# Optimization experiments

Measured on AMD Instinct MI355X. Metric: run time of the kernel, lower is better.

Reference implementation:

```python
import jax, jax.numpy as jnp
import numpy as np

HIDDEN = 256
NUM_CLASSES = 25
INPUT_DIM = 76


def _lstm_layer(x, Wi, Wh, b):
    """Flax OptimizedLSTMCell semantics: gates [i, f, g, o], zero-init carry.
    x: [B, T, D]; Wi: [D, 4H]; Wh: [H, 4H]; b: [4H]. Returns hidden seq [B, T, H]."""
    B = x.shape[0]
    H = Wh.shape[0]
    c0 = jnp.zeros((B, H), x.dtype)
    h0 = jnp.zeros((B, H), x.dtype)

    def step(carry, xt):
        c, h = carry
        z = xt @ Wi + h @ Wh + b  # [B, 4H]
        i, f, g, o = jnp.split(z, 4, axis=-1)
        i = jax.nn.sigmoid(i)
        f = jax.nn.sigmoid(f)
        g = jnp.tanh(g)
        o = jax.nn.sigmoid(o)
        c = f * c + i * g
        h = o * jnp.tanh(c)
        return (c, h), h

    (_, _), ys = jax.lax.scan(step, (c0, h0), jnp.swapaxes(x, 0, 1))  # scan over time
    return jnp.swapaxes(ys, 0, 1)  # [B, T, H]


def setup_inputs() -> dict:
    key = jax.random.key(0)
    ks = jax.random.split(key, 9)
    B, T, D, H = 512, 512, INPUT_DIM, HIDDEN
    s_in = 1.0 / np.sqrt(D)
    s_h = 1.0 / np.sqrt(H)
    return {
        "x": jax.random.normal(ks[0], (B, T, D), jnp.float32),
        "Wi1": jax.random.normal(ks[1], (D, 4 * H), jnp.float32) * s_in,
        "Wh1": jax.random.normal(ks[2], (H, 4 * H), jnp.float32) * s_h,
        "b1": jnp.zeros((4 * H,), jnp.float32),
        "Wi2": jax.random.normal(ks[3], (H, 4 * H), jnp.float32) * s_h,
        "Wh2": jax.random.normal(ks[4], (H, 4 * H), jnp.float32) * s_h,
        "b2": jnp.zeros((4 * H,), jnp.float32),
        "Wd": jax.random.normal(ks[5], (H, NUM_CLASSES), jnp.float32) * s_h,
        "bd": jnp.zeros((NUM_CLASSES,), jnp.float32),
    }


def reference(x, Wi1, Wh1, b1, Wi2, Wh2, b2, Wd, bd):
    h1 = _lstm_layer(x, Wi1, Wh1, b1)   # [B, T, H]
    h2 = _lstm_layer(h1, Wi2, Wh2, b2)  # [B, T, H]
    feats = h2[:, -1]                   # dropout deterministic (eval mode)
    logits = feats @ Wd + bd            # [B, num_classes]
    return logits
```

## Files before the change

kernel.cpp:

```cpp
#include <hip/hip_runtime.h>

#define BB 512
#define TT 512
#define DD 76
#define HH 256
#define NC 25
#define NBLK 256
#define NTHREADS 512
#define BBHH (BB * HH)

#define K1 352
#define K2 512
#define WS1 360
#define WS2 520

typedef unsigned short u16;
typedef unsigned int u32;
typedef unsigned long long u64;
typedef __attribute__((ext_vector_type(8))) short bf16x8;
typedef __attribute__((ext_vector_type(4))) float f32x4;

__device__ __forceinline__ float bf2f(u16 v) {
  union { u32 u; float f; } c; c.u = ((u32)v) << 16; return c.f;
}
__device__ __forceinline__ u16 f2bf(float f) {
  union { u32 u; float f; } c; c.f = f;
  u32 r = c.u + 0x7FFFu + ((c.u >> 16) & 1u);
  return (u16)(r >> 16);
}
__device__ __forceinline__ void split2(float f, u16& h, u16& l) {
  u16 hh = f2bf(f);
  float r = f - bf2f(hh);
  h = hh; l = f2bf(r);
}
__device__ __forceinline__ float tanh_f(float v) {
  float e = __expf(2.0f * v);
  return 1.0f - 2.0f / (e + 1.0f);
}
__device__ __forceinline__ float gact(float v, bool is_tanh) {
  float e = __expf(is_tanh ? 2.0f * v : -v);
  float inv = 1.0f / (1.0f + e);
  return is_tanh ? 1.0f - 2.0f * inv : inv;
}

__device__ __forceinline__ u64 ald2(const u32* p) {
  return __hip_atomic_load((const u64*)p, __ATOMIC_RELAXED, __HIP_MEMORY_SCOPE_AGENT);
}
__device__ __forceinline__ u32 ald1(const u32* p) {
  return __hip_atomic_load(p, __ATOMIC_RELAXED, __HIP_MEMORY_SCOPE_AGENT);
}
__device__ __forceinline__ void ast1(u32* p, u32 v) {
  __hip_atomic_store(p, v, __ATOMIC_RELAXED, __HIP_MEMORY_SCOPE_AGENT);
}
__device__ __forceinline__ void ast2(u64* p, u64 v) {
  __hip_atomic_store(p, v, __ATOMIC_RELAXED, __HIP_MEMORY_SCOPE_AGENT);
}

__device__ __forceinline__ void wait_flags(const u32* fbase, u32 target) {
  if (threadIdx.x < 32) {
    const u32* p = fbase + threadIdx.x * 32;
    while (__hip_atomic_load(p, __ATOMIC_RELAXED, __HIP_MEMORY_SCOPE_AGENT) < target)
      __builtin_amdgcn_s_sleep(1);
  }
  __syncthreads();
}
__device__ __forceinline__ void post_flag(u32* slot, u32 val) {
  __syncthreads();
  if (threadIdx.x == 0) ast1(slot, val);
}

__device__ __forceinline__ bf16x8 hi8(const u64 w[4]) {
  union { u32 u[4]; bf16x8 v; } c;
#pragma unroll
  for (int i = 0; i < 4; ++i)
    c.u[i] = __builtin_amdgcn_perm((u32)(w[i] >> 32), (u32)w[i], 0x05040100u);
  return c.v;
}
__device__ __forceinline__ bf16x8 lo8(const u64 w[4]) {
  union { u32 u[4]; bf16x8 v; } c;
#pragma unroll
  for (int i = 0; i < 4; ++i)
    c.u[i] = __builtin_amdgcn_perm((u32)(w[i] >> 32), (u32)w[i], 0x07060302u);
  return c.v;
}

__device__ __forceinline__ void splitv8(const float* f, bf16x8& vh, bf16x8& vl) {
  union { u16 s[8]; bf16x8 v; } ch, cl;
#pragma unroll
  for (int i = 0; i < 8; ++i) { u16 h_, l_; split2(f[i], h_, l_); ch.s[i] = h_; cl.s[i] = l_; }
  vh = ch.v; vl = cl.v;
}

__global__ void repack_kernel(const float* __restrict__ Wi1, const float* __restrict__ Wh1,
                              const float* __restrict__ Wi2, const float* __restrict__ Wh2,
                              u16* __restrict__ w1hg, u16* __restrict__ w1lg,
                              u16* __restrict__ w2hg, u16* __restrict__ w2lg) {
  int idx = blockIdx.x * blockDim.x + threadIdx.x;
  const int N1 = 1024 * K1;
  if (idx < N1) {
    int c = idx / K1, k = idx - c * K1;
    int src = (c & 3) * HH + (c >> 2);
    float v = 0.f;
    if (k < HH) v = Wh1[k * 1024 + src];
    else if (k < HH + DD) v = Wi1[(k - HH) * 1024 + src];
    u16 h, l; split2(v, h, l);
    w1hg[idx] = h; w1lg[idx] = l;
  } else if (idx < N1 + 1024 * K2) {
    int d = idx - N1;
    int c = d >> 9, k = d & 511;
    int src = (c & 3) * HH + (c >> 2);
    float v = (k < HH) ? Wi2[k * 1024 + src] : Wh2[(k - HH) * 1024 + src];
    u16 h, l; split2(v, h, l);
    w2hg[d] = h; w2lg[d] = l;
  }
}

#define MFMA_CH6(AH, AL, PH0, PL0, PH1, PL1, KOFF, A0, B0, C0, A1, B1, C1)  \
  { bf16x8 b0h_ = *(const bf16x8*)((PH0) + (KOFF));                         \
    bf16x8 b0l_ = *(const bf16x8*)((PL0) + (KOFF));                         \
    bf16x8 b1h_ = *(const bf16x8*)((PH1) + (KOFF));                         \
    bf16x8 b1l_ = *(const bf16x8*)((PL1) + (KOFF));                         \
    A0 = __builtin_amdgcn_mfma_f32_16x16x32_bf16(AH, b0h_, A0, 0, 0, 0);    \
    B0 = __builtin_amdgcn_mfma_f32_16x16x32_bf16(AH, b0l_, B0, 0, 0, 0);    \
    C0 = __builtin_amdgcn_mfma_f32_16x16x32_bf16(AL, b0h_, C0, 0, 0, 0);    \
    A1 = __builtin_amdgcn_mfma_f32_16x16x32_bf16(AH, b1h_, A1, 0, 0, 0);    \
    B1 = __builtin_amdgcn_mfma_f32_16x16x32_bf16(AH, b1l_, B1, 0, 0, 0);    \
    C1 = __builtin_amdgcn_mfma_f32_16x16x32_bf16(AL, b1h_, C1, 0, 0, 0); }

#define GATES_ST(Z, CS, DST)                                                \
  { u32 hwv[4];                                                             \
    _Pragma("unroll")                                                       \
    for (int r = 0; r < 4; ++r) {                                           \
      float a_ = gact((Z)[r], gi == 2);                                     \
      float v1_ = __shfl_xor(a_, 1);                                        \
      float v2_ = __shfl_xor(a_, 2);                                        \
      float v3_ = __shfl_xor(a_, 3);                                        \
      float cn_ = v1_ * (CS)[r] + a_ * v2_;                                 \
      (CS)[r] = cn_;                                                        \
      float hv_ = v3_ * tanh_f(cn_);                                        \
      u16 hh_, hl_; split2(hv_, hh_, hl_);                                  \
      hwv[r] = (u32)hh_ | ((u32)hl_ << 16);                                 \
    }                                                                       \
    _Pragma("unroll")                                                       \
    for (int r = 0; r < 4; ++r) {                                           \
      int base_ = lane & 48;                                                \
      u32 w1_ = __shfl(hwv[r], base_ + 4);                                  \
      u32 w2_ = __shfl(hwv[r], base_ + 8);                                  \
      u32 w3_ = __shfl(hwv[r], base_ + 12);                                 \
      if (nl == 0) {                                                        \
        u64* dp_ = (u64*)((DST) + (size_t)(rbase + r) * HH + jt * 8 + kh * 4); \
        ast2(dp_,     (u64)hwv[r] | ((u64)w1_ << 32));                      \
        ast2(dp_ + 1, (u64)w2_    | ((u64)w3_ << 32));                      \
      }                                                                     \
    }                                                                       \
  }

#define LOAD_RW(RW, BASEPTR)                                                \
  { const u32* hp_ = (BASEPTR) + (size_t)arow * HH + kh * 128;              \
    _Pragma("unroll")                                                       \
    for (int i_ = 0; i_ < 4; ++i_) {                                        \
      const u32* p_ = hp_ + i_ * 32 + qd * 8;                               \
      (RW)[i_][0] = ald2(p_);     (RW)[i_][1] = ald2(p_ + 2);               \
      (RW)[i_][2] = ald2(p_ + 4); (RW)[i_][3] = ald2(p_ + 6);               \
    } }

__global__ __launch_bounds__(NTHREADS) void lstm_kernel(
    const float* __restrict__ x,
    const float* __restrict__ b1, const float* __restrict__ b2,
    const float* __restrict__ Wd, const float* __restrict__ bd,
    const u16* __restrict__ w1hg, const u16* __restrict__ w1lg,
    const u16* __restrict__ w2hg, const u16* __restrict__ w2lg,
    u32* __restrict__ h1w, u32* __restrict__ h2w,
    u32* __restrict__ flags,
    float* __restrict__ out)
{
  __shared__ u16 w1h[32 * WS1], w1l[32 * WS1];
  __shared__ u16 w2h[32 * WS2], w2l[32 * WS2];
  __shared__ float zx[2][8][64][4];

  const int tid = threadIdx.x;
  const int lane = tid & 63;
  const int wv = tid >> 6;
  const int m  = wv & 3;
  const int kh = wv >> 2;
  const int nl = lane & 15;
  const int qd = lane >> 4;
  const int bt = blockIdx.x & 7;
  const int jt = blockIdx.x >> 3;
  const int row0 = bt * 64;

  u32* fCp = flags + bt * 1024;
  u32* fCslot = fCp + jt * 32;

  for (int i = tid; i < 32 * (K1 / 2); i += NTHREADS) {
    int c = i / 176, kk = i - c * 176;
    ((u32*)&w1h[c * WS1])[kk] = ((const u32*)(w1hg + (size_t)(jt * 32 + c) * K1))[kk];
    ((u32*)&w1l[c * WS1])[kk] = ((const u32*)(w1lg + (size_t)(jt * 32 + c) * K1))[kk];
  }
  for (int i = tid; i < 32 * (K2 / 2); i += NTHREADS) {
    int c = i >> 8, kk = i & 255;
    ((u32*)&w2h[c * WS2])[kk] = ((const u32*)(w2hg + (size_t)(jt * 32 + c) * K2))[kk];
    ((u32*)&w2l[c * WS2])[kk] = ((const u32*)(w2lg + (size_t)(jt * 32 + c) * K2))[kk];
  }

  const int cg_col = jt * 32 + kh * 16 + nl;
  const int gi = cg_col & 3;
  const int rbase = row0 + m * 16 + qd * 4;
  const int arow = row0 + m * 16 + nl;

  float ab1[2], ab2[2];
#pragma unroll
  for (int tl = 0; tl < 2; ++tl) {
    int col = jt * 32 + tl * 16 + nl;
    float v1 = b1[(col & 3) * HH + (col >> 2)];
    float v2 = b2[(col & 3) * HH + (col >> 2)];
    ab1[tl] = (kh == 0) ? v1 : 0.f;
    ab2[tl] = (kh == 0) ? v2 : 0.f;
  }

  const u16* pB1h0 = w1h + nl * WS1;
  const u16* pB1l0 = w1l + nl * WS1;
  const u16* pB1h1 = w1h + (16 + nl) * WS1;
  const u16* pB1l1 = w1l + (16 + nl) * WS1;
  const u16* pB2h0 = w2h + nl * WS2;
  const u16* pB2l0 = w2l + nl * WS2;
  const u16* pB2h1 = w2h + (16 + nl) * WS2;
  const u16* pB2l1 = w2l + (16 + nl) * WS2;

  float cs1[4] = {0.f, 0.f, 0.f, 0.f}, cs2[4] = {0.f, 0.f, 0.f, 0.f};
  u64 rwh1[4][4], rw2[4][4];

  __syncthreads();

  {
    f32x4 aA0 = {ab1[0], ab1[0], ab1[0], ab1[0]};
    f32x4 aA1 = {ab1[1], ab1[1], ab1[1], ab1[1]};
    f32x4 aB0 = {0,0,0,0}, aB1 = {0,0,0,0}, aC0 = {0,0,0,0}, aC1 = {0,0,0,0};
    const float* xrow = x + (size_t)arow * TT * DD;
    if (kh == 0) {
#pragma unroll
      for (int ci = 0; ci < 2; ++ci) {
        float xv[8];
        float4 f0 = *(const float4*)(xrow + ci * 32 + qd * 8);
        float4 f1 = *(const float4*)(xrow + ci * 32 + qd * 8 + 4);
        xv[0]=f0.x; xv[1]=f0.y; xv[2]=f0.z; xv[3]=f0.w;
        xv[4]=f1.x; xv[5]=f1.y; xv[6]=f1.z; xv[7]=f1.w;
        bf16x8 xh, xl; splitv8(xv, xh, xl);
        const int koff = (8 + ci) * 32 + qd * 8;
        MFMA_CH6(xh, xl, pB1h0, pB1l0, pB1h1, pB1l1, koff, aA0, aB0, aC0, aA1, aB1, aC1)
      }
    } else {
      float xv[8] = {0,0,0,0,0,0,0,0};
      if (qd == 0) {
        float4 f0 = *(const float4*)(xrow + 64);
        float4 f1 = *(const float4*)(xrow + 68);
        xv[0]=f0.x; xv[1]=f0.y; xv[2]=f0.z; xv[3]=f0.w;
        xv[4]=f1.x; xv[5]=f1.y; xv[6]=f1.z; xv[7]=f1.w;
      } else if (qd == 1) {
        float4 f0 = *(const float4*)(xrow + 72);
        xv[0]=f0.x; xv[1]=f0.y; xv[2]=f0.z; xv[3]=f0.w;
      }
      bf16x8 xh, xl; splitv8(xv, xh, xl);
      const int koff = 10 * 32 + qd * 8;
      MFMA_CH6(xh, xl, pB1h0, pB1l0, pB1h1, pB1l1, koff, aA0, aB0, aC0, aA1, aB1, aC1)
    }
    f32x4 zk = (kh == 0) ? (aA0 + aB0 + aC0) : (aA1 + aB1 + aC1);
    f32x4 zo = (kh == 0) ? (aA1 + aB1 + aC1) : (aA0 + aB0 + aC0);
    *(f32x4*)&zx[1][wv][lane][0] = zo;
    __syncthreads();
    zk += *(const f32x4*)&zx[1][wv ^ 4][lane][0];
    GATES_ST(zk, cs1, h1w)
    post_flag(fCslot, 1u);
  }

#pragma unroll 1
  for (int t = 0; t < TT; ++t) {
    const u32* h1cw = h1w + (t & 1) * BBHH;
    u32* h1nw = h1w + ((t + 1) & 1) * BBHH;
    const u32* h2pw = h2w + ((t + 1) & 1) * BBHH;
    u32* h2cw = h2w + (t & 1) * BBHH;
    const bool doA = (t < TT - 1);

    f32x4 aA0 = {ab1[0], ab1[0], ab1[0], ab1[0]};
    f32x4 aA1 = {ab1[1], ab1[1], ab1[1], ab1[1]};
    f32x4 aB0 = {0,0,0,0}, aB1 = {0,0,0,0}, aC0 = {0,0,0,0}, aC1 = {0,0,0,0};
    f32x4 bA0 = {ab2[0], ab2[0], ab2[0], ab2[0]};
    f32x4 bA1 = {ab2[1], ab2[1], ab2[1], ab2[1]};
    f32x4 bB0 = {0,0,0,0}, bB1 = {0,0,0,0}, bC0 = {0,0,0,0}, bC1 = {0,0,0,0};

    float4 xf0, xf1, xf2, xf3;
    if (doA) {
      const float* xrow = x + ((size_t)arow * TT + (t + 1)) * DD;
      if (kh == 0) {
        xf0 = *(const float4*)(xrow + qd * 8);
        xf1 = *(const float4*)(xrow + qd * 8 + 4);
        xf2 = *(const float4*)(xrow + 32 + qd * 8);
        xf3 = *(const float4*)(xrow + 32 + qd * 8 + 4);
      } else {
        xf0 = make_float4(0,0,0,0); xf1 = make_float4(0,0,0,0);
        if (qd == 0) {
          xf0 = *(const float4*)(xrow + 64);
          xf1 = *(const float4*)(xrow + 68);
        } else if (qd == 1) {
          xf0 = *(const float4*)(xrow + 72);
        }
      }
    }

    wait_flags(fCp, (u32)(t + 1));

    LOAD_RW(rwh1, h1cw)
    if (t > 0) LOAD_RW(rw2, h2pw)

    if (doA) {
      float xv[8]; bf16x8 xh, xl;
      if (kh == 0) {
        xv[0]=xf0.x; xv[1]=xf0.y; xv[2]=xf0.z; xv[3]=xf0.w;
        xv[4]=xf1.x; xv[5]=xf1.y; xv[6]=xf1.z; xv[7]=xf1.w;
        splitv8(xv, xh, xl);
        MFMA_CH6(xh, xl, pB1h0, pB1l0, pB1h1, pB1l1, 8 * 32 + qd * 8,
                 aA0, aB0, aC0, aA1, aB1, aC1)
        xv[0]=xf2.x; xv[1]=xf2.y; xv[2]=xf2.z; xv[3]=xf2.w;
        xv[4]=xf3.x; xv[5]=xf3.y; xv[6]=xf3.z; xv[7]=xf3.w;
        splitv8(xv, xh, xl);
        MFMA_CH6(xh, xl, pB1h0, pB1l0, pB1h1, pB1l1, 9 * 32 + qd * 8,
                 aA0, aB0, aC0, aA1, aB1, aC1)
      } else {
        xv[0]=xf0.x; xv[1]=xf0.y; xv[2]=xf0.z; xv[3]=xf0.w;
        xv[4]=xf1.x; xv[5]=xf1.y; xv[6]=xf1.z; xv[7]=xf1.w;
        splitv8(xv, xh, xl);
        MFMA_CH6(xh, xl, pB1h0, pB1l0, pB1h1, pB1l1, 10 * 32 + qd * 8,
                 aA0, aB0, aC0, aA1, aB1, aC1)
      }
    }

#pragma unroll
    for (int i = 0; i < 4; ++i) {
      bf16x8 fh = hi8(rwh1[i]), fl = lo8(rwh1[i]);
      const int koff = (kh * 4 + i) * 32 + qd * 8;
      if (doA)
        MFMA_CH6(fh, fl, pB1h0, pB1l0, pB1h1, pB1l1, koff, aA0, aB0, aC0, aA1, aB1, aC1)
      MFMA_CH6(fh, fl, pB2h0, pB2l0, pB2h1, pB2l1, koff, bA0, bB0, bC0, bA1, bB1, bC1)
    }
    if (t > 0) {
#pragma unroll
      for (int i = 0; i < 4; ++i) {
        bf16x8 fh = hi8(rw2[i]), fl = lo8(rw2[i]);
        const int koff = (8 + kh * 4 + i) * 32 + qd * 8;
        MFMA_CH6(fh, fl, pB2h0, pB2l0, pB2h1, pB2l1, koff, bA0, bB0, bC0, bA1, bB1, bC1)
      }
    }

    f32x4 z2k = (kh == 0) ? (bA0 + bB0 + bC0) : (bA1 + bB1 + bC1);
    f32x4 z2o = (kh == 0) ? (bA1 + bB1 + bC1) : (bA0 + bB0 + bC0);
    *(f32x4*)&zx[0][wv][lane][0] = z2o;
    f32x4 z1k = {0,0,0,0};
    if (doA) {
      z1k = (kh == 0) ? (aA0 + aB0 + aC0) : (aA1 + aB1 + aC1);
      f32x4 z1o = (kh == 0) ? (aA1 + aB1 + aC1) : (aA0 + aB0 + aC0);
      *(f32x4*)&zx[1][wv][lane][0] = z1o;
    }
    __syncthreads();
    z2k += *(const f32x4*)&zx[0][wv ^ 4][lane][0];
    if (doA) {
      z1k += *(const f32x4*)&zx[1][wv ^ 4][lane][0];
      GATES_ST(z1k, cs1, h1nw)
    }
    GATES_ST(z2k, cs2, h2cw)
    post_flag(fCslot, (u32)(t + 2));
  }

  wait_flags(fCp, TT + 1);
  if (tid < 2 * NC) {
    int r = row0 + jt * 2 + tid / NC;
    int n = tid - (tid / NC) * NC;
    float s = bd[n];
    const u32* fw = h2w + BBHH + (size_t)r * HH;
#pragma unroll 8
    for (int k = 0; k < HH; ++k) {
      u32 w = ald1(fw + k);
      s += (bf2f((u16)w) + bf2f((u16)(w >> 16))) * Wd[k * NC + n];
    }
    out[r * NC + n] = s;
  }
}

extern "C" void kernel_launch(void* const* d_in, const int* in_sizes, int n_in,
                              void* d_out, int out_size, void* d_ws, size_t ws_size,
                              hipStream_t stream) {
  const float* x   = (const float*)d_in[0];
  const float* Wi1 = (const float*)d_in[1];
  const float* Wh1 = (const float*)d_in[2];
  const float* b1  = (const float*)d_in[3];
  const float* Wi2 = (const float*)d_in[4];
  const float* Wh2 = (const float*)d_in[5];
  const float* b2  = (const float*)d_in[6];
  const float* Wd  = (const float*)d_in[7];
  const float* bd  = (const float*)d_in[8];

  char* ws = (char*)d_ws;
  u32* h1w = (u32*)(ws);
  u32* h2w = (u32*)(ws + 1048576u);
  u16* w1hg = (u16*)(ws + 2097152u);
  u16* w1lg = (u16*)(ws + 2097152u + 720896u);
  u16* w2hg = (u16*)(ws + 2097152u + 2u * 720896u);
  u16* w2lg = (u16*)(ws + 2097152u + 2u * 720896u + 1048576u);
  u32* flags = (u32*)(ws + 5636096u);
  float* out = (float*)d_out;

  hipMemsetAsync((void*)flags, 0, 65536, stream);
  const int total = 1024 * K1 + 1024 * K2;
  repack_kernel<<<(total + 255) / 256, 256, 0, stream>>>(
      Wi1, Wh1, Wi2, Wh2, w1hg, w1lg, w2hg, w2lg);

  void* args[] = {
    (void*)&x, (void*)&b1, (void*)&b2, (void*)&Wd, (void*)&bd,
    (void*)&w1hg, (void*)&w1lg, (void*)&w2hg, (void*)&w2lg,
    (void*)&h1w, (void*)&h2w,
    (void*)&flags, (void*)&out
  };
  (void)hipLaunchCooperativeKernel((void*)lstm_kernel, dim3(NBLK),
                                   dim3(NTHREADS), args, 0, stream);
}
```

Measured before the change: 5.481 ms.

## Split columns across waves instead of K to remove LDS reduction and barrier

Each wave now computes the full K reduction for one 16-column tile instead of half of K for two tiles. This removes the shared-memory partial-sum exchange and its __syncthreads. Every wave polls the inter-block flags itself, so the barrier after the wait is dropped. Before the flag is published, an explicit vmcnt wait ensures the h stores have completed. In exchange, each wave loads twice as many h values from global memory, holds more registers, and adds redundant flag polling.

```diff
diff --git a/kernel.cpp b/kernel.cpp
--- a/kernel.cpp
+++ b/kernel.cpp
@@ -56,17 +56,13 @@
   __hip_atomic_store(p, v, __ATOMIC_RELAXED, __HIP_MEMORY_SCOPE_AGENT);
 }
 
-__device__ __forceinline__ void wait_flags(const u32* fbase, u32 target) {
-  if (threadIdx.x < 32) {
-    const u32* p = fbase + threadIdx.x * 32;
+__device__ __forceinline__ void wwait(const u32* fbase, u32 target) {
+  if ((threadIdx.x & 63) < 32) {
+    const u32* p = fbase + (threadIdx.x & 63) * 32;
     while (__hip_atomic_load(p, __ATOMIC_RELAXED, __HIP_MEMORY_SCOPE_AGENT) < target)
       __builtin_amdgcn_s_sleep(1);
   }
-  __syncthreads();
-}
-__device__ __forceinline__ void post_flag(u32* slot, u32 val) {
-  __syncthreads();
-  if (threadIdx.x == 0) ast1(slot, val);
+  asm volatile("" ::: "memory");
 }
 
 __device__ __forceinline__ bf16x8 hi8(const u64 w[4]) {
@@ -85,10 +81,13 @@
 }
 
 __device__ __forceinline__ void splitv8(const float* f, bf16x8& vh, bf16x8& vl) {
-  union { u16 s[8]; bf16x8 v; } ch, cl;
-#pragma unroll
-  for (int i = 0; i < 8; ++i) { u16 h_, l_; split2(f[i], h_, l_); ch.s[i] = h_; cl.s[i] = l_; }
-  vh = ch.v; vl = cl.v;
+  union { u16 s[8]; bf16x8 v; } ch_, cl_;
+#pragma unroll
+  for (int i = 0; i < 8; ++i) {
+    u16 h_, l_; split2(f[i], h_, l_);
+    ch_.s[i] = h_; cl_.s[i] = l_;
+  }
+  vh = ch_.v; vl = cl_.v;
 }
 
 __global__ void repack_kernel(const float* __restrict__ Wi1, const float* __restrict__ Wh1,
@@ -115,17 +114,12 @@
   }
 }
 
-#define MFMA_CH6(AH, AL, PH0, PL0, PH1, PL1, KOFF, A0, B0, C0, A1, B1, C1)  \
-  { bf16x8 b0h_ = *(const bf16x8*)((PH0) + (KOFF));                         \
-    bf16x8 b0l_ = *(const bf16x8*)((PL0) + (KOFF));                         \
-    bf16x8 b1h_ = *(const bf16x8*)((PH1) + (KOFF));                         \
-    bf16x8 b1l_ = *(const bf16x8*)((PL1) + (KOFF));                         \
-    A0 = __builtin_amdgcn_mfma_f32_16x16x32_bf16(AH, b0h_, A0, 0, 0, 0);    \
-    B0 = __builtin_amdgcn_mfma_f32_16x16x32_bf16(AH, b0l_, B0, 0, 0, 0);    \
-    C0 = __builtin_amdgcn_mfma_f32_16x16x32_bf16(AL, b0h_, C0, 0, 0, 0);    \
-    A1 = __builtin_amdgcn_mfma_f32_16x16x32_bf16(AH, b1h_, A1, 0, 0, 0);    \
-    B1 = __builtin_amdgcn_mfma_f32_16x16x32_bf16(AH, b1l_, B1, 0, 0, 0);    \
-    C1 = __builtin_amdgcn_mfma_f32_16x16x32_bf16(AL, b1h_, C1, 0, 0, 0); }
+#define MCH3(AH, AL, PH, PL, KOFF, A, B, C)                                 \
+  { bf16x8 bh_ = *(const bf16x8*)((PH) + (KOFF));                           \
+    bf16x8 bl_ = *(const bf16x8*)((PL) + (KOFF));                           \
+    A = __builtin_amdgcn_mfma_f32_16x16x32_bf16(AH, bh_, A, 0, 0, 0);       \
+    B = __builtin_amdgcn_mfma_f32_16x16x32_bf16(AH, bl_, B, 0, 0, 0);       \
+    C = __builtin_amdgcn_mfma_f32_16x16x32_bf16(AL, bh_, C, 0, 0, 0); }
 
 #define GATES_ST(Z, CS, DST)                                                \
   { u32 hwv[4];                                                             \
@@ -148,21 +142,33 @@
       u32 w2_ = __shfl(hwv[r], base_ + 8);                                  \
       u32 w3_ = __shfl(hwv[r], base_ + 12);                                 \
       if (nl == 0) {                                                        \
-        u64* dp_ = (u64*)((DST) + (size_t)(rbase + r) * HH + jt * 8 + kh * 4); \
+        u64* dp_ = (u64*)((DST) + (size_t)(rbase + r) * HH + jt * 8 + ch * 4); \
         ast2(dp_,     (u64)hwv[r] | ((u64)w1_ << 32));                      \
         ast2(dp_ + 1, (u64)w2_    | ((u64)w3_ << 32));                      \
       }                                                                     \
     }                                                                       \
   }
 
-#define LOAD_RW(RW, BASEPTR)                                                \
-  { const u32* hp_ = (BASEPTR) + (size_t)arow * HH + kh * 128;              \
+#define LOAD_RW8(RW, BASEPTR)                                               \
+  { const u32* hp_ = (BASEPTR) + (size_t)arow * HH;                         \
     _Pragma("unroll")                                                       \
-    for (int i_ = 0; i_ < 4; ++i_) {                                        \
+    for (int i_ = 0; i_ < 8; ++i_) {                                        \
       const u32* p_ = hp_ + i_ * 32 + qd * 8;                               \
       (RW)[i_][0] = ald2(p_);     (RW)[i_][1] = ald2(p_ + 2);               \
       (RW)[i_][2] = ald2(p_ + 4); (RW)[i_][3] = ald2(p_ + 6);               \
     } }
+
+#define X_MFMA3(PH, PL, A, B, C)                                            \
+  { float xv[8]; bf16x8 xh, xl;                                             \
+    xv[0]=xa0.x; xv[1]=xa0.y; xv[2]=xa0.z; xv[3]=xa0.w;                     \
+    xv[4]=xa1.x; xv[5]=xa1.y; xv[6]=xa1.z; xv[7]=xa1.w;                     \
+    splitv8(xv, xh, xl); MCH3(xh, xl, PH, PL, 8 * 32 + qd * 8, A, B, C)     \
+    xv[0]=xb0.x; xv[1]=xb0.y; xv[2]=xb0.z; xv[3]=xb0.w;                     \
+    xv[4]=xb1.x; xv[5]=xb1.y; xv[6]=xb1.z; xv[7]=xb1.w;                     \
+    splitv8(xv, xh, xl); MCH3(xh, xl, PH, PL, 9 * 32 + qd * 8, A, B, C)     \
+    xv[0]=xc0.x; xv[1]=xc0.y; xv[2]=xc0.z; xv[3]=xc0.w;                     \
+    xv[4]=xc1.x; xv[5]=xc1.y; xv[6]=xc1.z; xv[7]=xc1.w;                     \
+    splitv8(xv, xh, xl); MCH3(xh, xl, PH, PL, 10 * 32 + qd * 8, A, B, C) }
 
 __global__ __launch_bounds__(NTHREADS) void lstm_kernel(
     const float* __restrict__ x,
@@ -176,13 +182,12 @@
 {
   __shared__ u16 w1h[32 * WS1], w1l[32 * WS1];
   __shared__ u16 w2h[32 * WS2], w2l[32 * WS2];
-  __shared__ float zx[2][8][64][4];
 
   const int tid = threadIdx.x;
   const int lane = tid & 63;
   const int wv = tid >> 6;
   const int m  = wv & 3;
-  const int kh = wv >> 2;
+  const int ch = wv >> 2;
   const int nl = lane & 15;
   const int qd = lane >> 4;
   const int bt = blockIdx.x & 7;
@@ -203,74 +208,42 @@
     ((u32*)&w2l[c * WS2])[kk] = ((const u32*)(w2lg + (size_t)(jt * 32 + c) * K2))[kk];
   }
 
-  const int cg_col = jt * 32 + kh * 16 + nl;
+  const int cg_col = jt * 32 + ch * 16 + nl;
   const int gi = cg_col & 3;
   const int rbase = row0 + m * 16 + qd * 4;
   const int arow = row0 + m * 16 + nl;
 
-  float ab1[2], ab2[2];
-#pragma unroll
-  for (int tl = 0; tl < 2; ++tl) {
-    int col = jt * 32 + tl * 16 + nl;
-    float v1 = b1[(col & 3) * HH + (col >> 2)];
-    float v2 = b2[(col & 3) * HH + (col >> 2)];
-    ab1[tl] = (kh == 0) ? v1 : 0.f;
-    ab2[tl] = (kh == 0) ? v2 : 0.f;
-  }
-
-  const u16* pB1h0 = w1h + nl * WS1;
-  const u16* pB1l0 = w1l + nl * WS1;
-  const u16* pB1h1 = w1h + (16 + nl) * WS1;
-  const u16* pB1l1 = w1l + (16 + nl) * WS1;
-  const u16* pB2h0 = w2h + nl * WS2;
-  const u16* pB2l0 = w2l + nl * WS2;
-  const u16* pB2h1 = w2h + (16 + nl) * WS2;
-  const u16* pB2l1 = w2l + (16 + nl) * WS2;
+  const float ab1 = b1[gi * HH + (cg_col >> 2)];
+  const float ab2 = b2[gi * HH + (cg_col >> 2)];
+
+  const u16* pB1h = w1h + (ch * 16 + nl) * WS1;
+  const u16* pB1l = w1l + (ch * 16 + nl) * WS1;
+  const u16* pB2h = w2h + (ch * 16 + nl) * WS2;
+  const u16* pB2l = w2l + (ch * 16 + nl) * WS2;
 
   float cs1[4] = {0.f, 0.f, 0.f, 0.f}, cs2[4] = {0.f, 0.f, 0.f, 0.f};
-  u64 rwh1[4][4], rw2[4][4];
+  u64 rwh1[8][4], rw2[8][4];
 
   __syncthreads();
 
   {
-    f32x4 aA0 = {ab1[0], ab1[0], ab1[0], ab1[0]};
-    f32x4 aA1 = {ab1[1], ab1[1], ab1[1], ab1[1]};
-    f32x4 aB0 = {0,0,0,0}, aB1 = {0,0,0,0}, aC0 = {0,0,0,0}, aC1 = {0,0,0,0};
+    f32x4 aA = {ab1, ab1, ab1, ab1};
+    f32x4 aB = {0,0,0,0}, aC = {0,0,0,0};
     const float* xrow = x + (size_t)arow * TT * DD;
-    if (kh == 0) {
-#pragma unroll
-      for (int ci = 0; ci < 2; ++ci) {
-        float xv[8];
-        float4 f0 = *(const float4*)(xrow + ci * 32 + qd * 8);
-        float4 f1 = *(const float4*)(xrow + ci * 32 + qd * 8 + 4);
-        xv[0]=f0.x; xv[1]=f0.y; xv[2]=f0.z; xv[3]=f0.w;
-        xv[4]=f1.x; xv[5]=f1.y; xv[6]=f1.z; xv[7]=f1.w;
-        bf16x8 xh, xl; splitv8(xv, xh, xl);
-        const int koff = (8 + ci) * 32 + qd * 8;
-        MFMA_CH6(xh, xl, pB1h0, pB1l0, pB1h1, pB1l1, koff, aA0, aB0, aC0, aA1, aB1, aC1)
-      }
-    } else {
-      float xv[8] = {0,0,0,0,0,0,0,0};
-      if (qd == 0) {
-        float4 f0 = *(const float4*)(xrow + 64);
-        float4 f1 = *(const float4*)(xrow + 68);
-        xv[0]=f0.x; xv[1]=f0.y; xv[2]=f0.z; xv[3]=f0.w;
-        xv[4]=f1.x; xv[5]=f1.y; xv[6]=f1.z; xv[7]=f1.w;
-      } else if (qd == 1) {
-        float4 f0 = *(const float4*)(xrow + 72);
-        xv[0]=f0.x; xv[1]=f0.y; xv[2]=f0.z; xv[3]=f0.w;
-      }
-      bf16x8 xh, xl; splitv8(xv, xh, xl);
-      const int koff = 10 * 32 + qd * 8;
-      MFMA_CH6(xh, xl, pB1h0, pB1l0, pB1h1, pB1l1, koff, aA0, aB0, aC0, aA1, aB1, aC1)
-    }
-    f32x4 zk = (kh == 0) ? (aA0 + aB0 + aC0) : (aA1 + aB1 + aC1);
-    f32x4 zo = (kh == 0) ? (aA1 + aB1 + aC1) : (aA0 + aB0 + aC0);
-    *(f32x4*)&zx[1][wv][lane][0] = zo;
+    float4 xa0 = *(const float4*)(xrow + qd * 8);
+    float4 xa1 = *(const float4*)(xrow + qd * 8 + 4);
+    float4 xb0 = *(const float4*)(xrow + 32 + qd * 8);
+    float4 xb1 = *(const float4*)(xrow + 32 + qd * 8 + 4);
+    float4 xc0 = make_float4(0,0,0,0), xc1 = make_float4(0,0,0,0);
+    if (qd == 0) { xc0 = *(const float4*)(xrow + 64);
+                   xc1 = *(const float4*)(xrow + 68); }
+    else if (qd == 1) { xc0 = *(const float4*)(xrow + 72); }
+    X_MFMA3(pB1h, pB1l, aA, aB, aC)
+    f32x4 z = aA + aB + aC;
+    GATES_ST(z, cs1, h1w)
+    asm volatile("s_waitcnt vmcnt(0)" ::: "memory");
     __syncthreads();
-    zk += *(const f32x4*)&zx[1][wv ^ 4][lane][0];
-    GATES_ST(zk, cs1, h1w)
-    post_flag(fCslot, 1u);
+    if (tid == 0) ast1(fCslot, 1u);
   }
 
 #pragma unroll 1
@@ -281,96 +254,61 @@
     u32* h2cw = h2w + (t & 1) * BBHH;
     const bool doA = (t < TT - 1);
 
-    f32x4 aA0 = {ab1[0], ab1[0], ab1[0], ab1[0]};
-    f32x4 aA1 = {ab1[1], ab1[1], ab1[1], ab1[1]};
-    f32x4 aB0 = {0,0,0,0}, aB1 = {0,0,0,0}, aC0 = {0,0,0,0}, aC1 = {0,0,0,0};
-    f32x4 bA0 = {ab2[0], ab2[0], ab2[0], ab2[0]};
-    f32x4 bA1 = {ab2[1], ab2[1], ab2[1], ab2[1]};
-    f32x4 bB0 = {0,0,0,0}, bB1 = {0,0,0,0}, bC0 = {0,0,0,0}, bC1 = {0,0,0,0};
-
-    float4 xf0, xf1, xf2, xf3;
+    f32x4 aA = {ab1, ab1, ab1, ab1};
+    f32x4 aB = {0,0,0,0}, aC = {0,0,0,0};
+    f32x4 bA = {ab2, ab2, ab2, ab2};
+    f32x4 bB = {0,0,0,0}, bC = {0,0,0,0};
+
+    float4 xa0, xa1, xb0, xb1, xc0, xc1;
     if (doA) {
       const float* xrow = x + ((size_t)arow * TT + (t + 1)) * DD;
-      if (kh == 0) {
-        xf0 = *(const float4*)(xrow + qd * 8);
-        xf1 = *(const float4*)(xrow + qd * 8 + 4);
-        xf2 = *(const float4*)(xrow + 32 + qd * 8);
-        xf3 = *(const float4*)(xrow + 32 + qd * 8 + 4);
-      } else {
-        xf0 = make_float4(0,0,0,0); xf1 = make_float4(0,0,0,0);
-        if (qd == 0) {
-          xf0 = *(const float4*)(xrow + 64);
-          xf1 = *(const float4*)(xrow + 68);
-        } else if (qd == 1) {
-          xf0 = *(const float4*)(xrow + 72);
-        }
+      xa0 = *(const float4*)(xrow + qd * 8);
+      xa1 = *(const float4*)(xrow + qd * 8 + 4);
+      xb0 = *(const float4*)(xrow + 32 + qd * 8);
+      xb1 = *(const float4*)(xrow + 32 + qd * 8 + 4);
+      xc0 = make_float4(0,0,0,0); xc1 = make_float4(0,0,0,0);
+      if (qd == 0) { xc0 = *(const float4*)(xrow + 64);
+                     xc1 = *(const float4*)(xrow + 68); }
+      else if (qd == 1) { xc0 = *(const float4*)(xrow + 72); }
+    }
+
+    wwait(fCp, (u32)(t + 1));
+
+    LOAD_RW8(rwh1, h1cw)
+    if (t > 0) LOAD_RW8(rw2, h2pw)
+
+    if (doA) {
+      X_MFMA3(pB1h, pB1l, aA, aB, aC)
+    }
+
+#pragma unroll
+    for (int i = 0; i < 8; ++i) {
+      bf16x8 fh = hi8(rwh1[i]), fl = lo8(rwh1[i]);
+      const int koff = i * 32 + qd * 8;
+      if (doA) MCH3(fh, fl, pB1h, pB1l, koff, aA, aB, aC)
+      MCH3(fh, fl, pB2h, pB2l, koff, bA, bB, bC)
+    }
+    if (t > 0) {
+#pragma unroll
+      for (int i = 0; i < 8; ++i) {
+        bf16x8 fh = hi8(rw2[i]), fl = lo8(rw2[i]);
+        MCH3(fh, fl, pB2h, pB2l, (8 + i) * 32 + qd * 8, bA, bB, bC)
       }
     }
 
-    wait_flags(fCp, (u32)(t + 1));
-
-    LOAD_RW(rwh1, h1cw)
-    if (t > 0) LOAD_RW(rw2, h2pw)
-
     if (doA) {
-      float xv[8]; bf16x8 xh, xl;
-      if (kh == 0) {
-        xv[0]=xf0.x; xv[1]=xf0.y; xv[2]=xf0.z; xv[3]=xf0.w;
-        xv[4]=xf1.x; xv[5]=xf1.y; xv[6]=xf1.z; xv[7]=xf1.w;
-        splitv8(xv, xh, xl);
-        MFMA_CH6(xh, xl, pB1h0, pB1l0, pB1h1, pB1l1, 8 * 32 + qd * 8,
-                 aA0, aB0, aC0, aA1, aB1, aC1)
-        xv[0]=xf2.x; xv[1]=xf2.y; xv[2]=xf2.z; xv[3]=xf2.w;
-        xv[4]=xf3.x; xv[5]=xf3.y; xv[6]=xf3.z; xv[7]=xf3.w;
-        splitv8(xv, xh, xl);
-        MFMA_CH6(xh, xl, pB1h0, pB1l0, pB1h1, pB1l1, 9 * 32 + qd * 8,
-                 aA0, aB0, aC0, aA1, aB1, aC1)
-      } else {
-        xv[0]=xf0.x; xv[1]=xf0.y; xv[2]=xf0.z; xv[3]=xf0.w;
-        xv[4]=xf1.x; xv[5]=xf1.y; xv[6]=xf1.z; xv[7]=xf1.w;
-        splitv8(xv, xh, xl);
-        MFMA_CH6(xh, xl, pB1h0, pB1l0, pB1h1, pB1l1, 10 * 32 + qd * 8,
-                 aA0, aB0, aC0, aA1, aB1, aC1)
-      }
-    }
-
-#pragma unroll
-    for (int i = 0; i < 4; ++i) {
-      bf16x8 fh = hi8(rwh1[i]), fl = lo8(rwh1[i]);
-      const int koff = (kh * 4 + i) * 32 + qd * 8;
-      if (doA)
-        MFMA_CH6(fh, fl, pB1h0, pB1l0, pB1h1, pB1l1, koff, aA0, aB0, aC0, aA1, aB1, aC1)
-      MFMA_CH6(fh, fl, pB2h0, pB2l0, pB2h1, pB2l1, koff, bA0, bB0, bC0, bA1, bB1, bC1)
-    }
-    if (t > 0) {
-#pragma unroll
-      for (int i = 0; i < 4; ++i) {
-        bf16x8 fh = hi8(rw2[i]), fl = lo8(rw2[i]);
-        const int koff = (8 + kh * 4 + i) * 32 + qd * 8;
-        MFMA_CH6(fh, fl, pB2h0, pB2l0, pB2h1, pB2l1, koff, bA0, bB0, bC0, bA1, bB1, bC1)
-      }
-    }
-
-    f32x4 z2k = (kh == 0) ? (bA0 + bB0 + bC0) : (bA1 + bB1 + bC1);
-    f32x4 z2o = (kh == 0) ? (bA1 + bB1 + bC1) : (bA0 + bB0 + bC0);
-    *(f32x4*)&zx[0][wv][lane][0] = z2o;
-    f32x4 z1k = {0,0,0,0};
-    if (doA) {
-      z1k = (kh == 0) ? (aA0 + aB0 + aC0) : (aA1 + aB1 + aC1);
-      f32x4 z1o = (kh == 0) ? (aA1 + aB1 + aC1) : (aA0 + aB0 + aC0);
-      *(f32x4*)&zx[1][wv][lane][0] = z1o;
-    }
+      f32x4 z1 = aA + aB + aC;
+      GATES_ST(z1, cs1, h1nw)
+    }
+    f32x4 z2 = bA + bB + bC;
+    GATES_ST(z2, cs2, h2cw)
+
+    asm volatile("s_waitcnt vmcnt(0)" ::: "memory");
     __syncthreads();
-    z2k += *(const f32x4*)&zx[0][wv ^ 4][lane][0];
-    if (doA) {
-      z1k += *(const f32x4*)&zx[1][wv ^ 4][lane][0];
-      GATES_ST(z1k, cs1, h1nw)
-    }
-    GATES_ST(z2k, cs2, h2cw)
-    post_flag(fCslot, (u32)(t + 2));
-  }
-
-  wait_flags(fCp, TT + 1);
+    if (tid == 0) ast1(fCslot, (u32)(t + 2));
+  }
+
+  wwait(fCp, TT + 1);
   if (tid < 2 * NC) {
     int r = row0 + jt * 2 + tid / NC;
     int n = tid - (tid / NC) * NC;
@@ -408,7 +346,7 @@
   u32* flags = (u32*)(ws + 5636096u);
   float* out = (float*)d_out;
 
-  hipMemsetAsync((void*)flags, 0, 65536, stream);
+  (void)hipMemsetAsync((void*)flags, 0, 65536, stream);
   const int total = 1024 * K1 + 1024 * K2;
   repack_kernel<<<(total + 255) / 256, 256, 0, stream>>>(
       Wi1, Wh1, Wi2, Wh2, w1hg, w1lg, w2hg, w2lg);
```

Measured after the change: 9.343 ms. 70.5% more time.

## Replace block barriers and per-block flags with wave-pair LDS flags and atomic counters

Applied to the files above, without the earlier changes.

Drops the __syncthreads-based post/wait and the 32 per-block flag slots that each group polled. Waves now sync pairwise through volatile LDS flags, and each 16-row slice synchronises across blocks on one global atomic counter per (batch tile, m), so a wave waits only on producers of its own rows. The partial-sum LDS buffer is double-buffered by step parity so it needs no trailing barrier. This cuts barrier and polling latency on the serial time loop, but it relies on hand-placed waitcnt and spin-waits whose memory ordering is delicate.

```diff
diff --git a/kernel.cpp b/kernel.cpp
--- a/kernel.cpp
+++ b/kernel.cpp
@@ -49,24 +49,8 @@
 __device__ __forceinline__ u32 ald1(const u32* p) {
   return __hip_atomic_load(p, __ATOMIC_RELAXED, __HIP_MEMORY_SCOPE_AGENT);
 }
-__device__ __forceinline__ void ast1(u32* p, u32 v) {
-  __hip_atomic_store(p, v, __ATOMIC_RELAXED, __HIP_MEMORY_SCOPE_AGENT);
-}
 __device__ __forceinline__ void ast2(u64* p, u64 v) {
   __hip_atomic_store(p, v, __ATOMIC_RELAXED, __HIP_MEMORY_SCOPE_AGENT);
-}
-
-__device__ __forceinline__ void wait_flags(const u32* fbase, u32 target) {
-  if (threadIdx.x < 32) {
-    const u32* p = fbase + threadIdx.x * 32;
-    while (__hip_atomic_load(p, __ATOMIC_RELAXED, __HIP_MEMORY_SCOPE_AGENT) < target)
-      __builtin_amdgcn_s_sleep(1);
-  }
-  __syncthreads();
-}
-__device__ __forceinline__ void post_flag(u32* slot, u32 val) {
-  __syncthreads();
-  if (threadIdx.x == 0) ast1(slot, val);
 }
 
 __device__ __forceinline__ bf16x8 hi8(const u64 w[4]) {
@@ -85,10 +69,13 @@
 }
 
 __device__ __forceinline__ void splitv8(const float* f, bf16x8& vh, bf16x8& vl) {
-  union { u16 s[8]; bf16x8 v; } ch, cl;
-#pragma unroll
-  for (int i = 0; i < 8; ++i) { u16 h_, l_; split2(f[i], h_, l_); ch.s[i] = h_; cl.s[i] = l_; }
-  vh = ch.v; vl = cl.v;
+  union { u16 s[8]; bf16x8 v; } ch_, cl_;
+#pragma unroll
+  for (int i = 0; i < 8; ++i) {
+    u16 h_, l_; split2(f[i], h_, l_);
+    ch_.s[i] = h_; cl_.s[i] = l_;
+  }
+  vh = ch_.v; vl = cl_.v;
 }
 
 __global__ void repack_kernel(const float* __restrict__ Wi1, const float* __restrict__ Wh1,
@@ -176,7 +163,11 @@
 {
   __shared__ u16 w1h[32 * WS1], w1l[32 * WS1];
   __shared__ u16 w2h[32 * WS2], w2l[32 * WS2];
-  __shared__ float zx[2][8][64][4];
+  __shared__ f32x4 zx[2][2][8][64];
+  __shared__ u32 epz[8], epd[4];
+
+  volatile u32* vepz = epz;
+  volatile u32* vepd = epd;
 
   const int tid = threadIdx.x;
   const int lane = tid & 63;
@@ -189,9 +180,10 @@
   const int jt = blockIdx.x >> 3;
   const int row0 = bt * 64;
 
-  u32* fCp = flags + bt * 1024;
-  u32* fCslot = fCp + jt * 32;
-
+  u32* cnt = flags + (bt * 4 + m) * 32;
+
+  if (tid < 8) epz[tid] = 0;
+  if (tid < 4) epd[tid] = 0;
   for (int i = tid; i < 32 * (K1 / 2); i += NTHREADS) {
     int c = i / 176, kk = i - c * 176;
     ((u32*)&w1h[c * WS1])[kk] = ((const u32*)(w1hg + (size_t)(jt * 32 + c) * K1))[kk];
@@ -266,11 +258,21 @@
     }
     f32x4 zk = (kh == 0) ? (aA0 + aB0 + aC0) : (aA1 + aB1 + aC1);
     f32x4 zo = (kh == 0) ? (aA1 + aB1 + aC1) : (aA0 + aB0 + aC0);
-    *(f32x4*)&zx[1][wv][lane][0] = zo;
-    __syncthreads();
-    zk += *(const f32x4*)&zx[1][wv ^ 4][lane][0];
+    zx[1][1][wv][lane] = zo;
+    asm volatile("s_waitcnt lgkmcnt(0)" ::: "memory");
+    vepz[wv] = 1u;
+    while (vepz[wv ^ 4] < 1u) __builtin_amdgcn_s_sleep(1);
+    __builtin_amdgcn_sched_barrier(0);
+    zk += zx[1][1][wv ^ 4][lane];
     GATES_ST(zk, cs1, h1w)
-    post_flag(fCslot, 1u);
+    asm volatile("s_waitcnt vmcnt(0)" ::: "memory");
+    if (kh == 1) {
+      vepd[m] = 1u;
+    } else {
+      while (vepd[m] < 1u) __builtin_amdgcn_s_sleep(1);
+      if (lane == 0)
+        __hip_atomic_fetch_add(cnt, 1u, __ATOMIC_RELAXED, __HIP_MEMORY_SCOPE_AGENT);
+    }
   }
 
 #pragma unroll 1
@@ -280,6 +282,7 @@
     const u32* h2pw = h2w + ((t + 1) & 1) * BBHH;
     u32* h2cw = h2w + (t & 1) * BBHH;
     const bool doA = (t < TT - 1);
+    const int pz = t & 1;
 
     f32x4 aA0 = {ab1[0], ab1[0], ab1[0], ab1[0]};
     f32x4 aA1 = {ab1[1], ab1[1], ab1[1], ab1[1]};
@@ -307,7 +310,12 @@
       }
     }
 
-    wait_flags(fCp, (u32)(t + 1));
+    {
+      const u32 tgt = 32u * (u32)(t + 1);
+      while (__hip_atomic_load(cnt, __ATOMIC_RELAXED, __HIP_MEMORY_SCOPE_AGENT) < tgt)
+        __builtin_amdgcn_s_sleep(1);
+      asm volatile("" ::: "memory");
+    }
 
     LOAD_RW(rwh1, h1cw)
     if (t > 0) LOAD_RW(rw2, h2pw)
@@ -353,25 +361,41 @@
 
     f32x4 z2k = (kh == 0) ? (bA0 + bB0 + bC0) : (bA1 + bB1 + bC1);
     f32x4 z2o = (kh == 0) ? (bA1 + bB1 + bC1) : (bA0 + bB0 + bC0);
-    *(f32x4*)&zx[0][wv][lane][0] = z2o;
     f32x4 z1k = {0,0,0,0};
+    zx[pz][0][wv][lane] = z2o;
     if (doA) {
       z1k = (kh == 0) ? (aA0 + aB0 + aC0) : (aA1 + aB1 + aC1);
       f32x4 z1o = (kh == 0) ? (aA1 + aB1 + aC1) : (aA0 + aB0 + aC0);
-      *(f32x4*)&zx[1][wv][lane][0] = z1o;
-    }
-    __syncthreads();
-    z2k += *(const f32x4*)&zx[0][wv ^ 4][lane][0];
+      zx[pz][1][wv][lane] = z1o;
+    }
+    asm volatile("s_waitcnt lgkmcnt(0)" ::: "memory");
+    vepz[wv] = (u32)(t + 2);
+    while (vepz[wv ^ 4] < (u32)(t + 2)) __builtin_amdgcn_s_sleep(1);
+    __builtin_amdgcn_sched_barrier(0);
+    z2k += zx[pz][0][wv ^ 4][lane];
     if (doA) {
-      z1k += *(const f32x4*)&zx[1][wv ^ 4][lane][0];
+      z1k += zx[pz][1][wv ^ 4][lane];
       GATES_ST(z1k, cs1, h1nw)
     }
     GATES_ST(z2k, cs2, h2cw)
-    post_flag(fCslot, (u32)(t + 2));
-  }
-
-  wait_flags(fCp, TT + 1);
+
+    asm volatile("s_waitcnt vmcnt(0)" ::: "memory");
+    if (kh == 1) {
+      vepd[m] = (u32)(t + 2);
+    } else {
+      while (vepd[m] < (u32)(t + 2)) __builtin_amdgcn_s_sleep(1);
+      if (lane == 0)
+        __hip_atomic_fetch_add(cnt, 1u, __ATOMIC_RELAXED, __HIP_MEMORY_SCOPE_AGENT);
+    }
+  }
+
   if (tid < 2 * NC) {
+    const int mh = jt >> 3;
+    u32* cnth = flags + (bt * 4 + mh) * 32;
+    const u32 tgt = 32u * (u32)(TT + 1);
+    while (__hip_atomic_load(cnth, __ATOMIC_RELAXED, __HIP_MEMORY_SCOPE_AGENT) < tgt)
+      __builtin_amdgcn_s_sleep(1);
+    asm volatile("" ::: "memory");
     int r = row0 + jt * 2 + tid / NC;
     int n = tid - (tid / NC) * NC;
     float s = bd[n];
@@ -408,7 +432,7 @@
   u32* flags = (u32*)(ws + 5636096u);
   float* out = (float*)d_out;
 
-  hipMemsetAsync((void*)flags, 0, 65536, stream);
+  (void)hipMemsetAsync((void*)flags, 0, 65536, stream);
   const int total = 1024 * K1 + 1024 * K2;
   repack_kernel<<<(total + 255) / 256, 256, 0, stream>>>(
       Wi1, Wh1, Wi2, Wh2, w1hg, w1lg, w2hg, w2lg);
```

New measurement: 9.915 ms. 1.81x slower.
